# Optimization experiments

Measured on AMD Instinct MI355X. Metric: run time of the kernel, lower is better.

The kernel has to match this reference:

```python
import jax, jax.numpy as jnp
import numpy as np

B, N, T_FULL, T, KS, FEAT = 32, 360, 512, 64, 8, 8
NLAYERS = 3   # DCGRU layers
GLAYERS = 4   # bidirectional GRU layers in GruKRegion


def _gru_layer(x, Wih, Whh, bih, bhh, reverse):
    # x: [M, Tg, in] -> [M, Tg, H]; PyTorch GRU gate order (r, z, n)
    M = x.shape[0]
    Hh = Whh.shape[1]
    xp = jnp.einsum('mti,gi->mtg', x, Wih) + bih  # precompute input projections
    if reverse:
        xp = xp[:, ::-1]

    def step(h, xg):
        gh = jnp.einsum('mh,gh->mg', h, Whh) + bhh
        xr, xz, xn = jnp.split(xg, 3, -1)
        hr, hz, hn = jnp.split(gh, 3, -1)
        r = jax.nn.sigmoid(xr + hr)
        z = jax.nn.sigmoid(xz + hz)
        n = jnp.tanh(xn + r * hn)
        hnew = (1.0 - z) * n + z * h
        return hnew, hnew

    _, hs = jax.lax.scan(step, jnp.zeros((M, Hh), x.dtype), jnp.swapaxes(xp, 0, 1))
    hs = jnp.swapaxes(hs, 0, 1)
    if reverse:
        hs = hs[:, ::-1]
    return hs


def _dcgru_cell(x, h, adj, gw, gb, cw, cb):
    # x, h: [B, N] (rnn_units = 1); adj: [B, N, N]; max_diffusion_step = 2
    def gconv(inp, st, W, bias):
        x0 = jnp.stack([inp, st], axis=-1)                     # [B,N,2]
        x1 = jnp.einsum('bnm,bmc->bnc', adj, x0)
        x2 = 2.0 * jnp.einsum('bnm,bmc->bnc', adj, x1) - x0    # Chebyshev recurrence
        # torch layout: [B,N,C,num_matrices] flattened channel-major
        xc = jnp.stack([x0, x1, x2], axis=-1).reshape(x0.shape[0], N, 6)
        return jnp.einsum('bnf,fo->bno', xc, W) + bias

    gates = jax.nn.sigmoid(gconv(x, h, gw, gb))                # [B,N,2]
    r, u = gates[..., 0], gates[..., 1]
    c = jnp.tanh(gconv(x, r * h, cw, cb)[..., 0])
    return u * h + (1.0 - u) * c


def _forward(full_seq, reconstruct_seq, node_feas, temperature,
             g0wih, g0whh, g0bih, g0bhh, gwih, gwhh, gbih, gbhh,
             l1w, l1b, l2w, l2b,
             enc_gw, enc_gb, enc_cw, enc_cb,
             dec_gw, dec_gb, dec_cw, dec_cb, proj_w, proj_b):
    b, n, tfull = full_seq.shape
    # ---- GruKRegion feature extractor ----
    x = full_seq.reshape(b * n, tfull // KS, KS)
    out = jnp.concatenate(
        [_gru_layer(x, g0wih[0], g0whh[0], g0bih[0], g0bhh[0], False),
         _gru_layer(x, g0wih[1], g0whh[1], g0bih[1], g0bhh[1], True)], axis=-1)
    for l in range(GLAYERS - 1):
        out = jnp.concatenate(
            [_gru_layer(out, gwih[l, 0], gwhh[l, 0], gbih[l, 0], gbhh[l, 0], False),
             _gru_layer(out, gwih[l, 1], gwhh[l, 1], gbih[l, 1], gbhh[l, 1], True)], axis=-1)
    feat = out[:, -1, :].reshape(b, n, 2 * KS)
    feat = jax.nn.leaky_relu(jnp.einsum('bnf,of->bno', feat, l1w) + l1b, 0.2)
    feat = jnp.einsum('bnf,of->bno', feat, l2w) + l2b          # [B,N,FEAT]
    # ---- Embed2GraphByProduct ----
    logits = jnp.einsum('bjk,bpk->bjp', feat, feat)            # [B,N,N]
    # ---- hard gumbel softmax ----
    U = jax.random.uniform(jax.random.key(42), logits.shape, logits.dtype)
    g = -jnp.log(-jnp.log(U + 1e-10) + 1e-10)
    y_soft = jax.nn.softmax((logits + g) / temperature, axis=-1)
    y_hard = jax.nn.one_hot(jnp.argmax(y_soft, -1), n, dtype=y_soft.dtype)
    adj = y_soft + jax.lax.stop_gradient(y_hard - y_soft)
    adj = jnp.where(jnp.eye(n, dtype=bool), 0.0, adj)          # zero diagonal
    # (original computes a random-walk matrix then discards it; skipped)
    # ---- encoder: scan over time, 3 stacked DCGRU layers ----
    seq = jnp.transpose(reconstruct_seq, (2, 0, 1))            # [T,B,N]

    def enc_step(hid, xt):
        o = xt
        new = []
        for l in range(NLAYERS):
            hnew = _dcgru_cell(o, hid[l], adj, enc_gw[l], enc_gb[l], enc_cw[l], enc_cb[l])
            new.append(hnew)
            o = hnew
        return jnp.stack(new), None

    hid, _ = jax.lax.scan(enc_step, jnp.zeros((NLAYERS, b, n), seq.dtype), seq)

    def dec_step(carry, _):
        hidc, inp = carry
        o = inp
        new = []
        for l in range(NLAYERS):
            hnew = _dcgru_cell(o, hidc[l], adj, dec_gw[l], dec_gb[l], dec_cw[l], dec_cb[l])
            new.append(hnew)
            o = hnew
        proj = o * proj_w[0, 0] + proj_b[0]                    # Linear(1,1)
        return (jnp.stack(new), proj), proj

    _, outs = jax.lax.scan(dec_step, (hid, jnp.zeros((b, n), seq.dtype)), None, length=T)
    return jnp.transpose(outs, (1, 2, 0))                      # [B,N,T]


def setup_inputs():
    key = jax.random.key(0)
    ks = jax.random.split(key, 24)
    s = 0.2
    p = lambda k, sh: jax.random.normal(k, sh, jnp.float32) * s
    return dict(
        full_seq=jax.random.normal(ks[0], (B, N, T_FULL), jnp.float32),
        reconstruct_seq=jax.random.normal(ks[1], (B, N, T), jnp.float32),
        node_feas=jax.random.normal(ks[2], (B, N, KS), jnp.float32),
        temperature=jnp.ones((), jnp.float32),
        g0wih=p(ks[3], (2, 3 * KS, KS)), g0whh=p(ks[4], (2, 3 * KS, KS)),
        g0bih=p(ks[5], (2, 3 * KS)), g0bhh=p(ks[6], (2, 3 * KS)),
        gwih=p(ks[7], (GLAYERS - 1, 2, 3 * KS, 2 * KS)),
        gwhh=p(ks[8], (GLAYERS - 1, 2, 3 * KS, KS)),
        gbih=p(ks[9], (GLAYERS - 1, 2, 3 * KS)), gbhh=p(ks[10], (GLAYERS - 1, 2, 3 * KS)),
        l1w=p(ks[11], (KS, 2 * KS)), l1b=p(ks[12], (KS,)),
        l2w=p(ks[13], (FEAT, KS)), l2b=p(ks[14], (FEAT,)),
        enc_gw=p(ks[15], (NLAYERS, 6, 2)), enc_gb=jnp.ones((NLAYERS, 2), jnp.float32),
        enc_cw=p(ks[16], (NLAYERS, 6, 1)), enc_cb=jnp.zeros((NLAYERS, 1), jnp.float32),
        dec_gw=p(ks[17], (NLAYERS, 6, 2)), dec_gb=jnp.ones((NLAYERS, 2), jnp.float32),
        dec_cw=p(ks[18], (NLAYERS, 6, 1)), dec_cb=jnp.zeros((NLAYERS, 1), jnp.float32),
        proj_w=p(ks[19], (1, 1)), proj_b=jnp.zeros((1,), jnp.float32),
    )


def reference(full_seq, reconstruct_seq, node_feas, temperature,
              g0wih, g0whh, g0bih, g0bhh, gwih, gwhh, gbih, gbhh,
              l1w, l1b, l2w, l2b,
              enc_gw, enc_gb, enc_cw, enc_cb,
              dec_gw, dec_gb, dec_cw, dec_cb, proj_w, proj_b):
    return _forward(full_seq, reconstruct_seq, node_feas, temperature,
                    g0wih, g0whh, g0bih, g0bhh, gwih, gwhh, gbih, gbhh,
                    l1w, l1b, l2w, l2b,
                    enc_gw, enc_gb, enc_cw, enc_cb,
                    dec_gw, dec_gb, dec_cw, dec_cb, proj_w, proj_b)
```

## Files before the change

kernel.cpp:

```cpp
#include <hip/hip_runtime.h>
#include <math.h>

#define M_SEQ 11520
#define NNODE 360
#define NB    32
#define TT    64

__device__ __forceinline__ float fsigd(float x)  { return 1.0f / (1.0f + __expf(-x)); }
__device__ __forceinline__ float ftanhd(float x) { return 1.0f - 2.0f / (__expf(2.0f * x) + 1.0f); }

__device__ __forceinline__ unsigned rotl32(unsigned x, int n) { return (x << n) | (x >> (32 - n)); }

__device__ __forceinline__ void tf2x32(unsigned& x0, unsigned& x1)
{
    const unsigned k0 = 0u, k1 = 42u, k2 = 0u ^ 42u ^ 0x1BD11BDAu;
    x0 += k0; x1 += k1;
#define R4(a,b,c,d) \
    x0 += x1; x1 = rotl32(x1,a); x1 ^= x0; \
    x0 += x1; x1 = rotl32(x1,b); x1 ^= x0; \
    x0 += x1; x1 = rotl32(x1,c); x1 ^= x0; \
    x0 += x1; x1 = rotl32(x1,d); x1 ^= x0;
    R4(13,15,26,6)   x0 += k1; x1 += k2 + 1u;
    R4(17,29,16,24)  x0 += k2; x1 += k0 + 2u;
    R4(13,15,26,6)   x0 += k0; x1 += k1 + 3u;
    R4(17,29,16,24)  x0 += k1; x1 += k2 + 4u;
    R4(13,15,26,6)   x0 += k2; x1 += k0 + 5u;
#undef R4
}

__device__ __forceinline__ float jax_uniform(unsigned idx)
{
    unsigned x0 = 0u, x1 = idx;
    tf2x32(x0, x1);
    unsigned bits = x0 ^ x1;
    return __uint_as_float((bits >> 9) | 0x3f800000u) - 1.0f;
}

template<int K>
__device__ __forceinline__ void swz_fma(float h, const float* w0, const float* w1,
                                        const float* w2, float& g0, float& g1, float& g2)
{
    float hk = __int_as_float(
        __builtin_amdgcn_ds_swizzle(__float_as_int(h), (K << 5) | 0x18));
    g0 += hk * w0[K];
    g1 += hk * w1[K];
    g2 += hk * w2[K];
    if constexpr (K < 7)
        swz_fma<K + 1>(h, w0, w1, w2, g0, g1, g2);
}

template<int I>
__device__ __forceinline__ void ldx(float* __restrict__ xv, const float* __restrict__ p)
{
    const float4* p4 = reinterpret_cast<const float4*>(p);
#pragma unroll
    for (int q = 0; q < I / 4; ++q) {
        float4 f = p4[q];
        xv[4*q] = f.x; xv[4*q+1] = f.y; xv[4*q+2] = f.z; xv[4*q+3] = f.w;
    }
}

template<int I>
__device__ __forceinline__ void xgates(const float* __restrict__ xv,
    const float* wx0, const float* wx1, const float* wx2,
    float bx0, float bx1, float bx2, float& xr, float& xz, float& xn)
{
    xr = bx0; xz = bx1; xn = bx2;
#pragma unroll
    for (int k = 0; k < I; ++k) {
        xr += xv[k] * wx0[k];
        xz += xv[k] * wx1[k];
        xn += xv[k] * wx2[k];
    }
}

__device__ __forceinline__ float hstep(float h, float xr, float xz, float xn,
    const float* w0, const float* w1, const float* w2,
    float bh0, float bh1, float bh2)
{
    float gh0 = bh0, gh1 = bh1, gh2 = bh2;
    swz_fma<0>(h, w0, w1, w2, gh0, gh1, gh2);
    float r  = fsigd(xr + gh0);
    float z  = fsigd(xz + gh1);
    float nn = ftanhd(xn + r * gh2);
    return (1.f - z) * nn + z * h;
}

template<int I>
__global__ __launch_bounds__(256) void gru_fused(
    const float* __restrict__ x,
    const float* __restrict__ wih,
    const float* __restrict__ whh,
    const float* __restrict__ bih,
    const float* __restrict__ bhh,
    float* __restrict__ out)
{
    const int tid = blockIdx.x * 256 + threadIdx.x;
    const int j   = tid & 7;
    const int md  = tid >> 3;
    if (md >= M_SEQ * 2) return;
    const int m = md >> 1, dir = md & 1;

    float wx0[I], wx1[I], wx2[I];
    const float* WI = wih + dir * 24 * I;
#pragma unroll
    for (int k = 0; k < I; ++k) {
        wx0[k] = WI[j * I + k];
        wx1[k] = WI[(8 + j) * I + k];
        wx2[k] = WI[(16 + j) * I + k];
    }
    float w0[8], w1[8], w2[8];
    const float* WH = whh + dir * 192;
#pragma unroll
    for (int k = 0; k < 8; ++k) {
        w0[k] = WH[j * 8 + k];
        w1[k] = WH[(8 + j) * 8 + k];
        w2[k] = WH[(16 + j) * 8 + k];
    }
    const float bx0 = bih[dir*24 + j], bx1 = bih[dir*24 + 8 + j], bx2 = bih[dir*24 + 16 + j];
    const float bh0 = bhh[dir*24 + j], bh1 = bhh[dir*24 + 8 + j], bh2 = bhh[dir*24 + 16 + j];

    const float* xm = x + (size_t)m * TT * I;
    float* om = out + (size_t)m * TT * 16 + dir * 8 + j;

    const int tstep = dir ? -1 : 1;
    const int tbase = dir ? TT - 1 : 0;

    float h = 0.f;
    float xva[I], xvb[I];
    ldx<I>(xva, xm + (tbase) * I);
    ldx<I>(xvb, xm + (tbase + tstep) * I);
    float cr, cz, cn;
    xgates<I>(xva, wx0, wx1, wx2, bx0, bx1, bx2, cr, cz, cn);

    for (int tt = 0; tt < TT; tt += 2) {
        const int t0 = tbase + tstep * tt;
        const int t1 = t0 + tstep;
        if (tt + 2 < TT) ldx<I>(xva, xm + (t0 + 2 * tstep) * I);
        float nr, nz, nn;
        xgates<I>(xvb, wx0, wx1, wx2, bx0, bx1, bx2, nr, nz, nn);
        h = hstep(h, cr, cz, cn, w0, w1, w2, bh0, bh1, bh2);
        om[t0 * 16] = h;
        if (tt + 3 < TT) ldx<I>(xvb, xm + (t0 + 3 * tstep) * I);
        h = hstep(h, nr, nz, nn, w0, w1, w2, bh0, bh1, bh2);
        om[t1 * 16] = h;
        xgates<I>(xva, wx0, wx1, wx2, bx0, bx1, bx2, cr, cz, cn);
    }
}

__global__ void feat_kernel(const float* __restrict__ gout,
                            const float* __restrict__ l1w, const float* __restrict__ l1b,
                            const float* __restrict__ l2w, const float* __restrict__ l2b,
                            float* __restrict__ feat)
{
    int m = blockIdx.x * blockDim.x + threadIdx.x;
    if (m >= M_SEQ) return;
    const float* xp = gout + (size_t)m * TT * 16 + (TT - 1) * 16;
    float xv[16];
#pragma unroll
    for (int i = 0; i < 16; ++i) xv[i] = xp[i];
    float h1[8];
#pragma unroll
    for (int o = 0; o < 8; ++o) {
        float a = 0.f;
#pragma unroll
        for (int f = 0; f < 16; ++f) a += xv[f] * l1w[o * 16 + f];
        a += l1b[o];
        h1[o] = (a >= 0.f) ? a : 0.2f * a;
    }
#pragma unroll
    for (int o = 0; o < 8; ++o) {
        float a = 0.f;
#pragma unroll
        for (int f = 0; f < 8; ++f) a += h1[f] * l2w[o * 8 + f];
        feat[(size_t)m * 8 + o] = a + l2b[o];
    }
}

__global__ void adj_kernel(const float* __restrict__ feat,
                           const float* __restrict__ tptr,
                           int* __restrict__ colp, float* __restrict__ vp)
{
    const int gw   = (blockIdx.x * blockDim.x + threadIdx.x) >> 6;
    const int lane = threadIdx.x & 63;
    if (gw >= NB * NNODE) return;
    const int b = gw / NNODE;
    const int n = gw - b * NNODE;
    const float T = tptr[0];
    const float* fb = feat + (size_t)b * NNODE * 8;
    float fn[8];
#pragma unroll
    for (int k = 0; k < 8; ++k) fn[k] = fb[(size_t)n * 8 + k];

    float sv[6];
    float mval = -3.0e38f; int midx = 1 << 30;
#pragma unroll
    for (int s = 0; s < 6; ++s) {
        int p = s * 64 + lane;
        float xs = -3.0e38f;
        if (p < NNODE) {
            const float* fp = fb + (size_t)p * 8;
            float d = 0.f;
#pragma unroll
            for (int k = 0; k < 8; ++k) d += fn[k] * fp[k];
            unsigned idx = (unsigned)gw * 360u + (unsigned)p;
            float u   = jax_uniform(idx);
            float gum = -logf(-logf(u + 1e-10f) + 1e-10f);
            xs = (d + gum) / T;
            if (xs > mval) { mval = xs; midx = p; }
        }
        sv[s] = xs;
    }
    for (int off = 32; off > 0; off >>= 1) {
        float ov = __shfl_xor(mval, off);
        int   oi = __shfl_xor(midx, off);
        if (ov > mval || (ov == mval && oi < midx)) { mval = ov; midx = oi; }
    }
    float ssum = 0.f;
#pragma unroll
    for (int s = 0; s < 6; ++s) {
        int p = s * 64 + lane;
        if (p < NNODE) ssum += expf(sv[s] - mval);
    }
    for (int off = 32; off > 0; off >>= 1) ssum += __shfl_xor(ssum, off);
    if (lane == 0) {
        float ys = 1.0f / ssum;
        float v  = ys + (1.0f - ys);
        if (midx == n) v = 0.0f;
        colp[gw] = midx;
        vp[gw]   = v;
    }
}

__device__ __forceinline__ void dc_layer(
    float o_own, float oa, float ob,
    float& hn, float ha, float hb,
    float v, float vv, int c1, int c2, bool act, int n,
    const float* __restrict__ W, float bgr, float bgu,
    const float* __restrict__ C, float cb,
    float* __restrict__ s_rh)
{
    float f1 = v * oa, f2 = vv * ob - o_own;
    float f4 = v * ha, f5 = vv * hb - hn;
    float r  = fsigd(o_own*W[0] + f1*W[2] + f2*W[4] + hn*W[6] + f4*W[8] + f5*W[10] + bgr);
    float rh = r * hn;
    if (act) s_rh[n] = rh;
    __syncthreads();
    float rha = s_rh[c1], rhb = s_rh[c2];
    float u  = fsigd(o_own*W[1] + f1*W[3] + f2*W[5] + hn*W[7] + f4*W[9] + f5*W[11] + bgu);
    float cnd = ftanhd(o_own*C[0] + f1*C[1] + f2*C[2] + rh*C[3]
                       + (v*rha)*C[4] + (vv*rhb - rh)*C[5] + cb);
    hn = u * hn + (1.f - u) * cnd;
}

__global__ __launch_bounds__(384, 1) void decode_kernel(
    const float* __restrict__ rec,
    const int*   __restrict__ colp, const float* __restrict__ vp,
    const float* __restrict__ egw, const float* __restrict__ egb,
    const float* __restrict__ ecw, const float* __restrict__ ecb,
    const float* __restrict__ dgw, const float* __restrict__ dgb,
    const float* __restrict__ dcw, const float* __restrict__ dcb,
    const float* __restrict__ pw,  const float* __restrict__ pb,
    float* __restrict__ outp)
{
    __shared__ float s_h[2][3][NNODE];
    __shared__ float s_x[2][NNODE];
    __shared__ float s_o[NNODE];
    __shared__ float s_rh[NNODE];
    __shared__ float s_v[NNODE];
    __shared__ int   s_c[NNODE];

    const int b = blockIdx.x;
    const int n = threadIdx.x;
    const bool act = n < NNODE;

    float inp0 = 0.f;
    if (act) {
        s_c[n] = colp[b * NNODE + n];
        s_v[n] = vp[b * NNODE + n];
        inp0   = rec[((size_t)b * NNODE + n) * TT + 0];
        s_h[0][0][n] = 0.f; s_h[0][1][n] = 0.f; s_h[0][2][n] = 0.f;
        s_x[0][n] = inp0;
    }
    __syncthreads();

    int c1 = 0, c2 = 0;
    float v = 0.f, vv = 0.f;
    if (act) {
        c1 = s_c[n];
        c2 = s_c[c1];
        v  = s_v[n];
        vv = 2.f * v * s_v[c1];
    }
    const float projw = pw[0], projb = pb[0];
    float hreg[3] = {0.f, 0.f, 0.f};

    float Wg[36], Bg[6], Wc[18], Cb[3];
#pragma unroll
    for (int k = 0; k < 36; ++k) Wg[k] = egw[k];
#pragma unroll
    for (int k = 0; k < 6;  ++k) Bg[k] = egb[k];
#pragma unroll
    for (int k = 0; k < 18; ++k) Wc[k] = ecw[k];
#pragma unroll
    for (int k = 0; k < 3;  ++k) Cb[k] = ecb[k];

    float o_own = inp0;
    int p = 0;
    for (int t = 0; t < TT; ++t) {
        float nx = (act && t + 1 < TT) ? rec[((size_t)b * NNODE + n) * TT + t + 1] : 0.f;
        float xa  = s_x[p][c1],    xb  = s_x[p][c2];
        float h0a = s_h[p][0][c1], h0b = s_h[p][0][c2];
        float h1a = s_h[p][1][c1], h1b = s_h[p][1][c2];
        float h2a = s_h[p][2][c1], h2b = s_h[p][2][c2];
        const int q = p ^ 1;
        dc_layer(o_own, xa, xb, hreg[0], h0a, h0b, v, vv, c1, c2, act, n,
                 Wg, Bg[0], Bg[1], Wc, Cb[0], s_rh);
        if (act) { s_h[q][0][n] = hreg[0]; s_o[n] = hreg[0]; }
        __syncthreads();
        float oa = s_o[c1], ob = s_o[c2];
        dc_layer(hreg[0], oa, ob, hreg[1], h1a, h1b, v, vv, c1, c2, act, n,
                 Wg + 12, Bg[2], Bg[3], Wc + 6, Cb[1], s_rh);
        if (act) { s_h[q][1][n] = hreg[1]; s_o[n] = hreg[1]; }
        __syncthreads();
        oa = s_o[c1]; ob = s_o[c2];
        dc_layer(hreg[1], oa, ob, hreg[2], h2a, h2b, v, vv, c1, c2, act, n,
                 Wg + 24, Bg[4], Bg[5], Wc + 12, Cb[2], s_rh);
        if (act) { s_h[q][2][n] = hreg[2]; s_x[q][n] = nx; }
        __syncthreads();
        o_own = nx; p = q;
    }

#pragma unroll
    for (int k = 0; k < 36; ++k) Wg[k] = dgw[k];
#pragma unroll
    for (int k = 0; k < 6;  ++k) Bg[k] = dgb[k];
#pragma unroll
    for (int k = 0; k < 18; ++k) Wc[k] = dcw[k];
#pragma unroll
    for (int k = 0; k < 3;  ++k) Cb[k] = dcb[k];

    float dinp = 0.f;
    for (int t = 0; t < TT; ++t) {
        float xa  = s_x[p][c1],    xb  = s_x[p][c2];
        float h0a = s_h[p][0][c1], h0b = s_h[p][0][c2];
        float h1a = s_h[p][1][c1], h1b = s_h[p][1][c2];
        float h2a = s_h[p][2][c1], h2b = s_h[p][2][c2];
        const int q = p ^ 1;
        dc_layer(dinp, xa, xb, hreg[0], h0a, h0b, v, vv, c1, c2, act, n,
                 Wg, Bg[0], Bg[1], Wc, Cb[0], s_rh);
        if (act) { s_h[q][0][n] = hreg[0]; s_o[n] = hreg[0]; }
        __syncthreads();
        float oa = s_o[c1], ob = s_o[c2];
        dc_layer(hreg[0], oa, ob, hreg[1], h1a, h1b, v, vv, c1, c2, act, n,
                 Wg + 12, Bg[2], Bg[3], Wc + 6, Cb[1], s_rh);
        if (act) { s_h[q][1][n] = hreg[1]; s_o[n] = hreg[1]; }
        __syncthreads();
        oa = s_o[c1]; ob = s_o[c2];
        dc_layer(hreg[1], oa, ob, hreg[2], h2a, h2b, v, vv, c1, c2, act, n,
                 Wg + 24, Bg[4], Bg[5], Wc + 12, Cb[2], s_rh);
        float proj = hreg[2] * projw + projb;
        if (act) {
            s_h[q][2][n] = hreg[2];
            s_x[q][n] = proj;
            outp[((size_t)b * NNODE + n) * TT + t] = proj;
        }
        __syncthreads();
        dinp = proj; p = q;
    }
}

extern "C" void kernel_launch(void* const* d_in, const int* in_sizes, int n_in,
                              void* d_out, int out_size, void* d_ws, size_t ws_size,
                              hipStream_t stream)
{
    (void)in_sizes; (void)n_in; (void)out_size; (void)ws_size;
    const float* full_seq = (const float*)d_in[0];
    const float* rec_seq  = (const float*)d_in[1];
    const float* temp     = (const float*)d_in[3];
    const float* g0wih    = (const float*)d_in[4];
    const float* g0whh    = (const float*)d_in[5];
    const float* g0bih    = (const float*)d_in[6];
    const float* g0bhh    = (const float*)d_in[7];
    const float* gwih     = (const float*)d_in[8];
    const float* gwhh     = (const float*)d_in[9];
    const float* gbih     = (const float*)d_in[10];
    const float* gbhh     = (const float*)d_in[11];
    const float* l1w      = (const float*)d_in[12];
    const float* l1b      = (const float*)d_in[13];
    const float* l2w      = (const float*)d_in[14];
    const float* l2b      = (const float*)d_in[15];
    const float* enc_gw   = (const float*)d_in[16];
    const float* enc_gb   = (const float*)d_in[17];
    const float* enc_cw   = (const float*)d_in[18];
    const float* enc_cb   = (const float*)d_in[19];
    const float* dec_gw   = (const float*)d_in[20];
    const float* dec_gb   = (const float*)d_in[21];
    const float* dec_cw   = (const float*)d_in[22];
    const float* dec_cb   = (const float*)d_in[23];
    const float* proj_w   = (const float*)d_in[24];
    const float* proj_b   = (const float*)d_in[25];
    float* outp = (float*)d_out;

    float* ws   = (float*)d_ws;
    float* feat = ws;
    float* vbuf = feat + (size_t)M_SEQ * 8;
    int*   cbuf = (int*)(vbuf + M_SEQ);
    float* bufA = (float*)(cbuf + M_SEQ);
    float* bufB = bufA + (size_t)M_SEQ * TT * 16;

    const int ggru = (M_SEQ * 2 * 8) / 256;
    gru_fused<8><<<ggru, 256, 0, stream>>>(full_seq, g0wih, g0whh, g0bih, g0bhh, bufA);
    gru_fused<16><<<ggru, 256, 0, stream>>>(bufA, gwih + 0 * 768, gwhh + 0 * 384,
                                            gbih + 0 * 48, gbhh + 0 * 48, bufB);
    gru_fused<16><<<ggru, 256, 0, stream>>>(bufB, gwih + 1 * 768, gwhh + 1 * 384,
                                            gbih + 1 * 48, gbhh + 1 * 48, bufA);
    gru_fused<16><<<ggru, 256, 0, stream>>>(bufA, gwih + 2 * 768, gwhh + 2 * 384,
                                            gbih + 2 * 48, gbhh + 2 * 48, bufB);
    feat_kernel<<<M_SEQ / 256, 256, 0, stream>>>(bufB, l1w, l1b, l2w, l2b, feat);
    adj_kernel<<<(NB * NNODE) / 4, 256, 0, stream>>>(feat, temp, cbuf, vbuf);
    decode_kernel<<<NB, 384, 0, stream>>>(rec_seq, cbuf, vbuf,
                                          enc_gw, enc_gb, enc_cw, enc_cb,
                                          dec_gw, dec_gb, dec_cw, dec_cb,
                                          proj_w, proj_b, outp);
}
```

Baseline: 527.5 us.

## Stage decoder sequence in LDS and store only last GRU timestep

The last GRU layer now writes only the timestep feat_kernel reads (index TT-1, which covers both directions), so most of its global stores are dropped. The decode kernel preloads the whole reconstruct sequence for its batch into a transposed shared-memory buffer with vectorized loads. It reuses that buffer to hold decoder outputs, replacing per-step global loads and stores with one coalesced write-back at the end. This removes the per-timestep global latency from the serial recurrence, at the cost of about 92KB of LDS per block and an extra final copy loop.

Measured after the change: 547.3 us. 3.8% more time.

```diff
diff --git a/kernel.cpp b/kernel.cpp
--- a/kernel.cpp
+++ b/kernel.cpp
@@ -86,7 +86,7 @@
     return (1.f - z) * nn + z * h;
 }
 
-template<int I>
+template<int I, bool LASTONLY>
 __global__ __launch_bounds__(256) void gru_fused(
     const float* __restrict__ x,
     const float* __restrict__ wih,
@@ -140,10 +140,10 @@
         float nr, nz, nn;
         xgates<I>(xvb, wx0, wx1, wx2, bx0, bx1, bx2, nr, nz, nn);
         h = hstep(h, cr, cz, cn, w0, w1, w2, bh0, bh1, bh2);
-        om[t0 * 16] = h;
+        if (!LASTONLY || t0 == TT - 1) om[t0 * 16] = h;
         if (tt + 3 < TT) ldx<I>(xvb, xm + (t0 + 3 * tstep) * I);
         h = hstep(h, nr, nz, nn, w0, w1, w2, bh0, bh1, bh2);
-        om[t1 * 16] = h;
+        if (!LASTONLY || t1 == TT - 1) om[t1 * 16] = h;
         xgates<I>(xva, wx0, wx1, wx2, bx0, bx1, bx2, cr, cz, cn);
     }
 }
@@ -263,8 +263,8 @@
     const float* __restrict__ pw,  const float* __restrict__ pb,
     float* __restrict__ outp)
 {
+    __shared__ float s_big[TT * 361];
     __shared__ float s_h[2][3][NNODE];
-    __shared__ float s_x[2][NNODE];
     __shared__ float s_o[NNODE];
     __shared__ float s_rh[NNODE];
     __shared__ float s_v[NNODE];
@@ -274,13 +274,20 @@
     const int n = threadIdx.x;
     const bool act = n < NNODE;
 
-    float inp0 = 0.f;
+    for (int f = threadIdx.x; f < (NNODE * TT) / 4; f += 384) {
+        const int nn = f >> 4;
+        const int t4 = (f & 15) << 2;
+        float4 r4 = *reinterpret_cast<const float4*>(
+            rec + ((size_t)b * NNODE + nn) * TT + t4);
+        s_big[(t4 + 0) * 361 + nn] = r4.x;
+        s_big[(t4 + 1) * 361 + nn] = r4.y;
+        s_big[(t4 + 2) * 361 + nn] = r4.z;
+        s_big[(t4 + 3) * 361 + nn] = r4.w;
+    }
     if (act) {
         s_c[n] = colp[b * NNODE + n];
         s_v[n] = vp[b * NNODE + n];
-        inp0   = rec[((size_t)b * NNODE + n) * TT + 0];
         s_h[0][0][n] = 0.f; s_h[0][1][n] = 0.f; s_h[0][2][n] = 0.f;
-        s_x[0][n] = inp0;
     }
     __syncthreads();
 
@@ -305,30 +312,34 @@
 #pragma unroll
     for (int k = 0; k < 3;  ++k) Cb[k] = ecb[k];
 
-    float o_own = inp0;
     int p = 0;
     for (int t = 0; t < TT; ++t) {
-        float nx = (act && t + 1 < TT) ? rec[((size_t)b * NNODE + n) * TT + t + 1] : 0.f;
-        float xa  = s_x[p][c1],    xb  = s_x[p][c2];
-        float h0a = s_h[p][0][c1], h0b = s_h[p][0][c2];
-        float h1a = s_h[p][1][c1], h1b = s_h[p][1][c2];
-        float h2a = s_h[p][2][c1], h2b = s_h[p][2][c2];
+        const float* row = s_big + t * 361;
+        float o_own=0.f, xa=0.f, xb=0.f;
+        float h0a=0.f,h0b=0.f,h1a=0.f,h1b=0.f,h2a=0.f,h2b=0.f;
+        if (act) {
+            o_own = row[n]; xa = row[c1]; xb = row[c2];
+            h0a = s_h[p][0][c1]; h0b = s_h[p][0][c2];
+            h1a = s_h[p][1][c1]; h1b = s_h[p][1][c2];
+            h2a = s_h[p][2][c1]; h2b = s_h[p][2][c2];
+        }
         const int q = p ^ 1;
         dc_layer(o_own, xa, xb, hreg[0], h0a, h0b, v, vv, c1, c2, act, n,
                  Wg, Bg[0], Bg[1], Wc, Cb[0], s_rh);
         if (act) { s_h[q][0][n] = hreg[0]; s_o[n] = hreg[0]; }
         __syncthreads();
-        float oa = s_o[c1], ob = s_o[c2];
+        float oa = 0.f, ob = 0.f;
+        if (act) { oa = s_o[c1]; ob = s_o[c2]; }
         dc_layer(hreg[0], oa, ob, hreg[1], h1a, h1b, v, vv, c1, c2, act, n,
                  Wg + 12, Bg[2], Bg[3], Wc + 6, Cb[1], s_rh);
         if (act) { s_h[q][1][n] = hreg[1]; s_o[n] = hreg[1]; }
         __syncthreads();
-        oa = s_o[c1]; ob = s_o[c2];
+        if (act) { oa = s_o[c1]; ob = s_o[c2]; }
         dc_layer(hreg[1], oa, ob, hreg[2], h2a, h2b, v, vv, c1, c2, act, n,
                  Wg + 24, Bg[4], Bg[5], Wc + 12, Cb[2], s_rh);
-        if (act) { s_h[q][2][n] = hreg[2]; s_x[q][n] = nx; }
-        __syncthreads();
-        o_own = nx; p = q;
+        if (act) s_h[q][2][n] = hreg[2];
+        __syncthreads();
+        p = q;
     }
 
 #pragma unroll
@@ -342,31 +353,43 @@
 
     float dinp = 0.f;
     for (int t = 0; t < TT; ++t) {
-        float xa  = s_x[p][c1],    xb  = s_x[p][c2];
-        float h0a = s_h[p][0][c1], h0b = s_h[p][0][c2];
-        float h1a = s_h[p][1][c1], h1b = s_h[p][1][c2];
-        float h2a = s_h[p][2][c1], h2b = s_h[p][2][c2];
+        float xa=0.f, xb=0.f;
+        float h0a=0.f,h0b=0.f,h1a=0.f,h1b=0.f,h2a=0.f,h2b=0.f;
+        if (act) {
+            if (t > 0) {
+                const float* prow = s_big + (t - 1) * 361;
+                xa = prow[c1]; xb = prow[c2];
+            }
+            h0a = s_h[p][0][c1]; h0b = s_h[p][0][c2];
+            h1a = s_h[p][1][c1]; h1b = s_h[p][1][c2];
+            h2a = s_h[p][2][c1]; h2b = s_h[p][2][c2];
+        }
         const int q = p ^ 1;
         dc_layer(dinp, xa, xb, hreg[0], h0a, h0b, v, vv, c1, c2, act, n,
                  Wg, Bg[0], Bg[1], Wc, Cb[0], s_rh);
         if (act) { s_h[q][0][n] = hreg[0]; s_o[n] = hreg[0]; }
         __syncthreads();
-        float oa = s_o[c1], ob = s_o[c2];
+        float oa = 0.f, ob = 0.f;
+        if (act) { oa = s_o[c1]; ob = s_o[c2]; }
         dc_layer(hreg[0], oa, ob, hreg[1], h1a, h1b, v, vv, c1, c2, act, n,
                  Wg + 12, Bg[2], Bg[3], Wc + 6, Cb[1], s_rh);
         if (act) { s_h[q][1][n] = hreg[1]; s_o[n] = hreg[1]; }
         __syncthreads();
-        oa = s_o[c1]; ob = s_o[c2];
+        if (act) { oa = s_o[c1]; ob = s_o[c2]; }
         dc_layer(hreg[1], oa, ob, hreg[2], h2a, h2b, v, vv, c1, c2, act, n,
                  Wg + 24, Bg[4], Bg[5], Wc + 12, Cb[2], s_rh);
         float proj = hreg[2] * projw + projb;
         if (act) {
             s_h[q][2][n] = hreg[2];
-            s_x[q][n] = proj;
-            outp[((size_t)b * NNODE + n) * TT + t] = proj;
+            s_big[t * 361 + n] = proj;
         }
         __syncthreads();
         dinp = proj; p = q;
+    }
+
+    for (int e = threadIdx.x; e < NNODE * TT; e += 384) {
+        const int nn = e >> 6, t2 = e & 63;
+        outp[((size_t)b * NNODE + nn) * TT + t2] = s_big[t2 * 361 + nn];
     }
 }
 
@@ -410,13 +433,13 @@
     float* bufB = bufA + (size_t)M_SEQ * TT * 16;
 
     const int ggru = (M_SEQ * 2 * 8) / 256;
-    gru_fused<8><<<ggru, 256, 0, stream>>>(full_seq, g0wih, g0whh, g0bih, g0bhh, bufA);
-    gru_fused<16><<<ggru, 256, 0, stream>>>(bufA, gwih + 0 * 768, gwhh + 0 * 384,
-                                            gbih + 0 * 48, gbhh + 0 * 48, bufB);
-    gru_fused<16><<<ggru, 256, 0, stream>>>(bufB, gwih + 1 * 768, gwhh + 1 * 384,
-                                            gbih + 1 * 48, gbhh + 1 * 48, bufA);
-    gru_fused<16><<<ggru, 256, 0, stream>>>(bufA, gwih + 2 * 768, gwhh + 2 * 384,
-                                            gbih + 2 * 48, gbhh + 2 * 48, bufB);
+    gru_fused<8,false><<<ggru, 256, 0, stream>>>(full_seq, g0wih, g0whh, g0bih, g0bhh, bufA);
+    gru_fused<16,false><<<ggru, 256, 0, stream>>>(bufA, gwih + 0 * 768, gwhh + 0 * 384,
+                                                  gbih + 0 * 48, gbhh + 0 * 48, bufB);
+    gru_fused<16,false><<<ggru, 256, 0, stream>>>(bufB, gwih + 1 * 768, gwhh + 1 * 384,
+                                                  gbih + 1 * 48, gbhh + 1 * 48, bufA);
+    gru_fused<16,true><<<ggru, 256, 0, stream>>>(bufA, gwih + 2 * 768, gwhh + 2 * 384,
+                                                 gbih + 2 * 48, gbhh + 2 * 48, bufB);
     feat_kernel<<<M_SEQ / 256, 256, 0, stream>>>(bufB, l1w, l1b, l2w, l2b, feat);
     adj_kernel<<<(NB * NNODE) / 4, 256, 0, stream>>>(feat, temp, cbuf, vbuf);
     decode_kernel<<<NB, 384, 0, stream>>>(rec_seq, cbuf, vbuf,
```
